# Performance work log

Measured on AMD Instinct MI355X. Metric: run time of the kernel, lower is better.

## Reference

```python
import jax, jax.numpy as jnp
import numpy as np

EPS = 1e-12

def _l2norm(v, axis):
    # matches torch F.normalize: divide by norm clamped to eps
    n = jnp.sqrt(jnp.sum(v * v, axis=axis, keepdims=True))
    return v / jnp.maximum(n, EPS)

def setup_inputs() -> dict:
    key = jax.random.key(0)
    k1, k2 = jax.random.split(key)
    B, C, S, D = 256, 1000, 4, 512
    x = jax.random.normal(k1, (B, D), dtype=jnp.float32)
    # xavier_uniform over [C, S, D]: fan_in = S*D? torch treats dims (S, D) pairwise; approximate with uniform bound
    bound = float(np.sqrt(6.0 / (S + D)))
    W = jax.random.uniform(k2, (C, S, D), dtype=jnp.float32, minval=-bound, maxval=bound)
    return {"x": x, "W": W}

def reference(x, W):
    xn = _l2norm(x, axis=1)            # [B, D]
    Wn = _l2norm(W, axis=2)            # [C, S, D]
    logits = jnp.einsum('bd,csd->bcs', xn, Wn)        # [B, C, S]
    x_proj = jnp.einsum('bcs,csd->bcd', logits, Wn)   # [B, C, D]
    x_proj = _l2norm(x_proj, axis=2)
    out = jnp.einsum('bd,bcd->bc', xn, x_proj)        # [B, C]
    return out
```

## Files before the change

### kernel.cpp

```cpp
#include <hip/hip_runtime.h>

#define B_ 256
#define C_ 1000
#define D_ 512

typedef __bf16 bf16x8 __attribute__((ext_vector_type(8)));
typedef float  f32x4  __attribute__((ext_vector_type(4)));

__device__ __forceinline__ bf16x8 cvt8(float4 a, float4 b) {
    bf16x8 r;
    r[0] = (__bf16)a.x; r[1] = (__bf16)a.y; r[2] = (__bf16)a.z; r[3] = (__bf16)a.w;
    r[4] = (__bf16)b.x; r[5] = (__bf16)b.y; r[6] = (__bf16)b.z; r[7] = (__bf16)b.w;
    return r;
}

__global__ __launch_bounds__(256) void k_pack(const float* __restrict__ x,
                                              const float* __restrict__ W,
                                              __bf16* __restrict__ Wf,
                                              __bf16* __restrict__ xf,
                                              float* __restrict__ invx) {
    int blk = blockIdx.x;
    int t = threadIdx.x;
    if (blk < 1000) {
        int n = blk * 256 + t;
        int r = n >> 6;
        int j = n & 63;
        const float* src = W + r * D_ + j * 8;
        float4 a = *(const float4*)src;
        float4 b = *(const float4*)(src + 4);
        int ct = r >> 4, l15 = r & 15, ks = j >> 2, quad = j & 3;
        int idx = ((ct * 16 + ks) * 4 + quad) * 16 + l15;
        *(bf16x8*)(Wf + idx * 8) = cvt8(a, b);
    } else {
        int n = (blk - 1000) * 256 + t;
        int r = n >> 6;
        int j = n & 63;
        const float* src = x + r * D_ + j * 8;
        float4 a = *(const float4*)src;
        float4 b = *(const float4*)(src + 4);
        int bt = r >> 4, l15 = r & 15, ks = j >> 2, quad = j & 3;
        int idx = ((bt * 16 + ks) * 4 + quad) * 16 + l15;
        *(bf16x8*)(xf + idx * 8) = cvt8(a, b);
        float sn = a.x*a.x + a.y*a.y + a.z*a.z + a.w*a.w
                 + b.x*b.x + b.y*b.y + b.z*b.z + b.w*b.w;
        #pragma unroll
        for (int o = 32; o; o >>= 1) sn += __shfl_down(sn, o);
        if ((t & 63) == 0) invx[r] = 1.0f / fmaxf(sqrtf(sn), 1e-12f);
    }
}

__global__ __launch_bounds__(256) void k_main(const __bf16* __restrict__ Wf,
                                              const __bf16* __restrict__ xf,
                                              const float* __restrict__ invx,
                                              float* __restrict__ out) {
    int blk = blockIdx.x;
    int ct = blk >> 2;
    int bg = blk & 3;
    int t = threadIdx.x;
    int lane = t & 63, wv = t >> 6;
    int l15 = lane & 15, quad = lane >> 4;
    int bt = bg * 4 + wv;

    const bf16x8* A = (const bf16x8*)Wf + (ct * 64 + quad) * 16 + l15;
    const bf16x8* Bp = (const bf16x8*)xf + (bt * 64 + quad) * 16 + l15;

    f32x4 acc_l = {0.f, 0.f, 0.f, 0.f};
    f32x4 acc_g = {0.f, 0.f, 0.f, 0.f};
    #pragma unroll
    for (int ks = 0; ks < 16; ks++) {
        bf16x8 af = A[ks * 64];
        bf16x8 bf = Bp[ks * 64];
        acc_l = __builtin_amdgcn_mfma_f32_16x16x32_bf16(af, bf, acc_l, 0, 0, 0);
        acc_g = __builtin_amdgcn_mfma_f32_16x16x32_bf16(af, af, acc_g, 0, 0, 0);
    }

    float ivx = invx[bt * 16 + l15];

    float g[4][4];
    #pragma unroll
    for (int s = 0; s < 4; s++) {
        float v = acc_g[s];
        #pragma unroll
        for (int q = 0; q < 4; q++) g[s][q] = __shfl(v, 20 * quad + q);
    }

    float iv[4], l[4];
    #pragma unroll
    for (int s = 0; s < 4; s++) iv[s] = 1.0f / fmaxf(sqrtf(fmaxf(g[s][s], 0.f)), 1e-12f);
    #pragma unroll
    for (int s = 0; s < 4; s++) l[s] = acc_l[s] * ivx * iv[s];

    float num = l[0]*l[0] + l[1]*l[1] + l[2]*l[2] + l[3]*l[3];
    float den2 = 0.f;
    #pragma unroll
    for (int s = 0; s < 4; s++) {
        float r = 0.f;
        #pragma unroll
        for (int q = 0; q < 4; q++) r += g[s][q] * iv[q] * l[q];
        den2 += l[s] * iv[s] * r;
    }
    float den = fmaxf(sqrtf(fmaxf(den2, 0.f)), 1e-12f);
    float val = num / den;

    float4 o;
    o.x = __shfl(val, l15);
    o.y = __shfl(val, l15 + 16);
    o.z = __shfl(val, l15 + 32);
    o.w = __shfl(val, l15 + 48);
    if (quad == 0)
        *(float4*)(out + (bt * 16 + l15) * C_ + ct * 4) = o;
}

extern "C" void kernel_launch(void* const* d_in, const int* in_sizes, int n_in,
                              void* d_out, int out_size, void* d_ws, size_t ws_size,
                              hipStream_t stream) {
    const float* x = (const float*)d_in[0];
    const float* W = (const float*)d_in[1];
    float* out = (float*)d_out;

    char* ws = (char*)d_ws;
    __bf16* Wf  = (__bf16*)ws;
    __bf16* xf  = (__bf16*)(ws + 8192000);
    float*  ivx = (float*)(ws + 8192000 + 524288);

    k_pack<<<1064, 256, 0, stream>>>(x, W, Wf, xf, ivx);
    k_main<<<1000, 256, 0, stream>>>(Wf, xf, ivx, out);
}
```

Before: 69.80 us.

## Fuse W bf16 conversion into main kernel via LDS staging

Drops the separate pass that converts W to a packed bf16 buffer in global memory. The main kernel now loads its 16-row fp32 W tile, converts it to bf16 into shared memory in MFMA fragment order, and reuses that tile across two batch tiles per wave. The grid is halved to 500 blocks so each block covers half the batch. This removes the 8 MB bf16 write and re-read, and the Gram MFMA is computed once per wave instead of once per batch tile. In exchange it adds an LDS round trip and a __syncthreads, and only 500 blocks are launched.

Result: no change. 69.16 us (-0.9%).

```diff
diff --git a/kernel.cpp b/kernel.cpp
--- a/kernel.cpp
+++ b/kernel.cpp
@@ -4,6 +4,7 @@
 #define C_ 1000
 #define D_ 512
 
+typedef __bf16 bf16x4 __attribute__((ext_vector_type(4)));
 typedef __bf16 bf16x8 __attribute__((ext_vector_type(8)));
 typedef float  f32x4  __attribute__((ext_vector_type(4)));
 
@@ -13,102 +14,112 @@
     r[4] = (__bf16)b.x; r[5] = (__bf16)b.y; r[6] = (__bf16)b.z; r[7] = (__bf16)b.w;
     return r;
 }
-
-__global__ __launch_bounds__(256) void k_pack(const float* __restrict__ x,
-                                              const float* __restrict__ W,
-                                              __bf16* __restrict__ Wf,
-                                              __bf16* __restrict__ xf,
-                                              float* __restrict__ invx) {
-    int blk = blockIdx.x;
-    int t = threadIdx.x;
-    if (blk < 1000) {
-        int n = blk * 256 + t;
-        int r = n >> 6;
-        int j = n & 63;
-        const float* src = W + r * D_ + j * 8;
-        float4 a = *(const float4*)src;
-        float4 b = *(const float4*)(src + 4);
-        int ct = r >> 4, l15 = r & 15, ks = j >> 2, quad = j & 3;
-        int idx = ((ct * 16 + ks) * 4 + quad) * 16 + l15;
-        *(bf16x8*)(Wf + idx * 8) = cvt8(a, b);
-    } else {
-        int n = (blk - 1000) * 256 + t;
-        int r = n >> 6;
-        int j = n & 63;
-        const float* src = x + r * D_ + j * 8;
-        float4 a = *(const float4*)src;
-        float4 b = *(const float4*)(src + 4);
-        int bt = r >> 4, l15 = r & 15, ks = j >> 2, quad = j & 3;
-        int idx = ((bt * 16 + ks) * 4 + quad) * 16 + l15;
-        *(bf16x8*)(xf + idx * 8) = cvt8(a, b);
-        float sn = a.x*a.x + a.y*a.y + a.z*a.z + a.w*a.w
-                 + b.x*b.x + b.y*b.y + b.z*b.z + b.w*b.w;
-        #pragma unroll
-        for (int o = 32; o; o >>= 1) sn += __shfl_down(sn, o);
-        if ((t & 63) == 0) invx[r] = 1.0f / fmaxf(sqrtf(sn), 1e-12f);
-    }
+__device__ __forceinline__ bf16x4 cvt4(float4 a) {
+    bf16x4 r;
+    r[0] = (__bf16)a.x; r[1] = (__bf16)a.y; r[2] = (__bf16)a.z; r[3] = (__bf16)a.w;
+    return r;
 }
 
-__global__ __launch_bounds__(256) void k_main(const __bf16* __restrict__ Wf,
-                                              const __bf16* __restrict__ xf,
-                                              const float* __restrict__ invx,
-                                              float* __restrict__ out) {
+__global__ __launch_bounds__(256) void k_packx(const float* __restrict__ x,
+                                               __bf16* __restrict__ xf,
+                                               float* __restrict__ invx) {
+    int n = blockIdx.x * 256 + threadIdx.x;
+    int r = n >> 6;
+    int j = n & 63;
+    const float* src = x + r * D_ + j * 8;
+    float4 a = *(const float4*)src;
+    float4 b = *(const float4*)(src + 4);
+    int bt = r >> 4, l15 = r & 15, ks = j >> 2, quad = j & 3;
+    int idx = ((bt * 16 + ks) * 4 + quad) * 16 + l15;
+    *(bf16x8*)(xf + idx * 8) = cvt8(a, b);
+    float sn = a.x*a.x + a.y*a.y + a.z*a.z + a.w*a.w
+             + b.x*b.x + b.y*b.y + b.z*b.z + b.w*b.w;
+    #pragma unroll
+    for (int o = 32; o; o >>= 1) sn += __shfl_down(sn, o);
+    if ((threadIdx.x & 63) == 0) invx[r] = 1.0f / fmaxf(sqrtf(sn), 1e-12f);
+}
+
+__global__ __launch_bounds__(256, 2) void k_main(const float* __restrict__ W,
+                                                 const __bf16* __restrict__ xf,
+                                                 const float* __restrict__ invx,
+                                                 float* __restrict__ out) {
+    __shared__ __align__(16) char smem[64 * 272];
     int blk = blockIdx.x;
-    int ct = blk >> 2;
-    int bg = blk & 3;
+    int ct = blk >> 1;
+    int bh = blk & 1;
     int t = threadIdx.x;
     int lane = t & 63, wv = t >> 6;
     int l15 = lane & 15, quad = lane >> 4;
-    int bt = bg * 4 + wv;
 
-    const bf16x8* A = (const bf16x8*)Wf + (ct * 64 + quad) * 16 + l15;
-    const bf16x8* Bp = (const bf16x8*)xf + (bt * 64 + quad) * 16 + l15;
+    const float* wbase = W + ct * 16 * D_;
+    #pragma unroll
+    for (int p = 0; p < 8; p++) {
+        int ch = t + 256 * p;
+        int row = ch >> 7, pos = ch & 127;
+        float4 v = *(const float4*)(wbase + row * D_ + pos * 4);
+        int ks = pos >> 3, qd = (pos >> 1) & 3, off = (pos & 1) * 4;
+        *(bf16x4*)(smem + (ks * 4 + qd) * 272 + row * 16 + off * 2) = cvt4(v);
+    }
+    __syncthreads();
 
-    f32x4 acc_l = {0.f, 0.f, 0.f, 0.f};
-    f32x4 acc_g = {0.f, 0.f, 0.f, 0.f};
+    int bt0 = bh * 8 + wv * 2;
+    int bt1 = bt0 + 1;
+    const bf16x8* xp0 = (const bf16x8*)xf + (bt0 * 64 + quad) * 16 + l15;
+    const bf16x8* xp1 = (const bf16x8*)xf + (bt1 * 64 + quad) * 16 + l15;
+    const char* lp = smem + quad * 272 + l15 * 16;
+
+    f32x4 acc0 = {0.f, 0.f, 0.f, 0.f};
+    f32x4 acc1 = {0.f, 0.f, 0.f, 0.f};
+    f32x4 accg = {0.f, 0.f, 0.f, 0.f};
     #pragma unroll
     for (int ks = 0; ks < 16; ks++) {
-        bf16x8 af = A[ks * 64];
-        bf16x8 bf = Bp[ks * 64];
-        acc_l = __builtin_amdgcn_mfma_f32_16x16x32_bf16(af, bf, acc_l, 0, 0, 0);
-        acc_g = __builtin_amdgcn_mfma_f32_16x16x32_bf16(af, af, acc_g, 0, 0, 0);
+        bf16x8 af = *(const bf16x8*)(lp + ks * 1088);
+        bf16x8 b0 = xp0[ks * 64];
+        bf16x8 b1 = xp1[ks * 64];
+        acc0 = __builtin_amdgcn_mfma_f32_16x16x32_bf16(af, b0, acc0, 0, 0, 0);
+        acc1 = __builtin_amdgcn_mfma_f32_16x16x32_bf16(af, b1, acc1, 0, 0, 0);
+        accg = __builtin_amdgcn_mfma_f32_16x16x32_bf16(af, af, accg, 0, 0, 0);
     }
-
-    float ivx = invx[bt * 16 + l15];
 
     float g[4][4];
     #pragma unroll
     for (int s = 0; s < 4; s++) {
-        float v = acc_g[s];
+        float v = accg[s];
         #pragma unroll
         for (int q = 0; q < 4; q++) g[s][q] = __shfl(v, 20 * quad + q);
     }
-
-    float iv[4], l[4];
+    float iv[4];
     #pragma unroll
     for (int s = 0; s < 4; s++) iv[s] = 1.0f / fmaxf(sqrtf(fmaxf(g[s][s], 0.f)), 1e-12f);
+
     #pragma unroll
-    for (int s = 0; s < 4; s++) l[s] = acc_l[s] * ivx * iv[s];
+    for (int sub = 0; sub < 2; sub++) {
+        int bt = sub ? bt1 : bt0;
+        f32x4 acc = sub ? acc1 : acc0;
+        float ivx = invx[bt * 16 + l15];
+        float l[4];
+        #pragma unroll
+        for (int s = 0; s < 4; s++) l[s] = acc[s] * ivx * iv[s];
+        float num = l[0]*l[0] + l[1]*l[1] + l[2]*l[2] + l[3]*l[3];
+        float den2 = 0.f;
+        #pragma unroll
+        for (int s = 0; s < 4; s++) {
+            float r = 0.f;
+            #pragma unroll
+            for (int q = 0; q < 4; q++) r += g[s][q] * iv[q] * l[q];
+            den2 += l[s] * iv[s] * r;
+        }
+        float den = fmaxf(sqrtf(fmaxf(den2, 0.f)), 1e-12f);
+        float val = num / den;
 
-    float num = l[0]*l[0] + l[1]*l[1] + l[2]*l[2] + l[3]*l[3];
-    float den2 = 0.f;
-    #pragma unroll
-    for (int s = 0; s < 4; s++) {
-        float r = 0.f;
-        #pragma unroll
-        for (int q = 0; q < 4; q++) r += g[s][q] * iv[q] * l[q];
-        den2 += l[s] * iv[s] * r;
+        float4 o;
+        o.x = __shfl(val, l15);
+        o.y = __shfl(val, l15 + 16);
+        o.z = __shfl(val, l15 + 32);
+        o.w = __shfl(val, l15 + 48);
+        if (quad == 0)
+            *(float4*)(out + (bt * 16 + l15) * C_ + ct * 4) = o;
     }
-    float den = fmaxf(sqrtf(fmaxf(den2, 0.f)), 1e-12f);
-    float val = num / den;
-
-    float4 o;
-    o.x = __shfl(val, l15);
-    o.y = __shfl(val, l15 + 16);
-    o.z = __shfl(val, l15 + 32);
-    o.w = __shfl(val, l15 + 48);
-    if (quad == 0)
-        *(float4*)(out + (bt * 16 + l15) * C_ + ct * 4) = o;
 }
 
 extern "C" void kernel_launch(void* const* d_in, const int* in_sizes, int n_in,
@@ -119,10 +130,9 @@
     float* out = (float*)d_out;
 
     char* ws = (char*)d_ws;
-    __bf16* Wf  = (__bf16*)ws;
-    __bf16* xf  = (__bf16*)(ws + 8192000);
-    float*  ivx = (float*)(ws + 8192000 + 524288);
+    __bf16* xf  = (__bf16*)ws;
+    float*  ivx = (float*)(ws + 524288);
 
-    k_pack<<<1064, 256, 0, stream>>>(x, W, Wf, xf, ivx);
-    k_main<<<1000, 256, 0, stream>>>(Wf, xf, ivx, out);
+    k_packx<<<64, 256, 0, stream>>>(x, xf, ivx);
+    k_main<<<500, 256, 0, stream>>>(W, xf, ivx, out);
 }
```
